# Optimization experiments

Measured on AMD Instinct MI355X. Metric: run time of the kernel, lower is better.

The kernel has to match this reference:

```python
import jax, jax.numpy as jnp
import numpy as np

NEG_SLOPE = 0.2  # PyG GATConv default LeakyReLU slope


def _gat_layer(x, src, dst, W, a_src, a_dst, b, n_nodes):
    # x: [N, Fin]; W: [Fin, H*C]; a_src/a_dst: [H, C]; b: [H*C]
    H, C = a_src.shape
    h = (x @ W).reshape(n_nodes, H, C)            # [N,H,C]
    e_s = jnp.einsum('nhc,hc->nh', h, a_src)      # [N,H]
    e_d = jnp.einsum('nhc,hc->nh', h, a_dst)
    e = jax.nn.leaky_relu(e_s[src] + e_d[dst], NEG_SLOPE)   # [E,H]
    # segment softmax over edges grouped by destination node
    m = jax.ops.segment_max(e, dst, num_segments=n_nodes)   # [N,H]
    ex = jnp.exp(e - m[dst])
    denom = jax.ops.segment_sum(ex, dst, num_segments=n_nodes)
    coef = ex / denom[dst]                         # [E,H]
    out = jax.ops.segment_sum(h[src] * coef[:, :, None], dst, num_segments=n_nodes)
    return out.reshape(n_nodes, H * C) + b         # concat=True


def _xavier(key, shape):
    fan_in, fan_out = shape[0], shape[-1]
    lim = float(np.sqrt(6.0 / (fan_in + fan_out)))
    return jax.random.uniform(key, shape, jnp.float32, -lim, lim)


def setup_inputs() -> dict:
    key = jax.random.key(0)
    ks = jax.random.split(key, 24)
    N, E, Fin, G = 50000, 1600000, 128, 64
    x = jax.random.normal(ks[0], (N, Fin), jnp.float32)
    edge_index = jax.random.randint(ks[1], (2, E), 0, N, jnp.int64)
    batch = jnp.sort(jax.random.randint(ks[2], (N,), 0, G, jnp.int64))
    # (Fin, H, C) per layer
    cfg = [(128, 1, 32), (32, 2, 32), (64, 2, 64), (128, 2, 32), (64, 2, 8)]
    params = {}
    i = 3
    for li, (fi, H, C) in enumerate(cfg, 1):
        params[f'W{li}'] = _xavier(ks[i], (fi, H * C)); i += 1
        params[f'as{li}'] = _xavier(ks[i], (H, C)) ; i += 1
        params[f'ad{li}'] = _xavier(ks[i], (H, C)) ; i += 1
        params[f'b{li}'] = jnp.zeros((H * C,), jnp.float32)
    params['fcW'] = _xavier(ks[20], (16, 1))
    params['fcb'] = jnp.zeros((1,), jnp.float32)
    return dict(x=x, edge_index=edge_index, batch=batch, **params)


def reference(x, edge_index, batch,
              W1, as1, ad1, b1, W2, as2, ad2, b2, W3, as3, ad3, b3,
              W4, as4, ad4, b4, W5, as5, ad5, b5, fcW, fcb):
    N = x.shape[0]
    G = 64
    # add self-loops (PyG GATConv default add_self_loops=True)
    loop = jnp.arange(N, dtype=edge_index.dtype)
    src = jnp.concatenate([edge_index[0], loop])
    dst = jnp.concatenate([edge_index[1], loop])
    h = jax.nn.relu(_gat_layer(x, src, dst, W1, as1, ad1, b1, N))
    h = jax.nn.relu(_gat_layer(h, src, dst, W2, as2, ad2, b2, N))
    h = jax.nn.relu(_gat_layer(h, src, dst, W3, as3, ad3, b3, N))
    h = jax.nn.relu(_gat_layer(h, src, dst, W4, as4, ad4, b4, N))
    h = jax.nn.relu(_gat_layer(h, src, dst, W5, as5, ad5, b5, N))
    # global mean pool over graphs (dropout is identity at inference)
    sums = jax.ops.segment_sum(h, batch, num_segments=G)          # [G,16]
    cnt = jax.ops.segment_sum(jnp.ones((N,), h.dtype), batch, num_segments=G)
    pooled = sums / jnp.maximum(cnt, 1.0)[:, None]
    return jax.nn.sigmoid(pooled @ fcW + fcb)                     # [G,1]
```

## Files before the change

kernel.cpp:

```cpp
#include <hip/hip_runtime.h>
#include <math.h>

#define TPB 256
#define NEG_SLOPE 0.2f
#define EPB 2048
#define BK 512

static inline int cdiv_l(long a, int b){ return (int)((a + b - 1) / b); }

typedef float v2f __attribute__((ext_vector_type(2)));

__device__ __forceinline__ ushort f2bf(float f){
  unsigned u = __float_as_uint(f);
  unsigned r = u + 0x7fffu + ((u >> 16) & 1u);
  return (ushort)(r >> 16);
}
__device__ __forceinline__ float bf2f(unsigned hi16){ return __uint_as_float(hi16 << 16); }
__device__ __forceinline__ unsigned pbf2(float a, float b){
  return (unsigned)f2bf(a) | ((unsigned)f2bf(b) << 16);
}

template<int Fin, int HC, int C, typename XT>
__global__ __launch_bounds__(256) void gemm2_k(const XT* __restrict__ X,
        const float* __restrict__ W, const float* __restrict__ as_,
        const float* __restrict__ ad_, float* __restrict__ es, float* __restrict__ ed,
        unsigned char* __restrict__ Hb, int N){
  constexpr int TPN = HC / 4;
  constexpr int NPB = 256 / TPN;
  constexpr int H   = HC / C;
  constexpr int RG  = C / 4;
  __shared__ float Wl[Fin * HC];
  for (int i = threadIdx.x; i < Fin * HC; i += 256) Wl[i] = W[i];
  __syncthreads();
  const int t  = threadIdx.x;
  const int n  = blockIdx.x * NPB + t / TPN;
  const int jt = (t % TPN) * 4;
  if (n >= N) return;
  const XT* xr = X + (size_t)n * Fin;
  float acc[4] = {0.f, 0.f, 0.f, 0.f};
  for (int k = 0; k < Fin; k += 4){
    float xv[4];
    if constexpr (sizeof(XT) == 4){
      float4 v = *(const float4*)(xr + k);
      xv[0] = v.x; xv[1] = v.y; xv[2] = v.z; xv[3] = v.w;
    } else {
      uint2 u = *(const uint2*)(xr + k);
      xv[0] = bf2f(u.x & 0xffffu); xv[1] = bf2f(u.x >> 16);
      xv[2] = bf2f(u.y & 0xffffu); xv[3] = bf2f(u.y >> 16);
    }
#pragma unroll
    for (int kk = 0; kk < 4; ++kk){
#pragma unroll
      for (int j = 0; j < 4; ++j)
        acc[j] = fmaf(xv[kk], Wl[(k + kk) * HC + jt + j], acc[j]);
    }
  }
  int pk8 = __builtin_amdgcn_cvt_pk_fp8_f32(acc[0], acc[1], 0, false);
  pk8     = __builtin_amdgcn_cvt_pk_fp8_f32(acc[2], acc[3], pk8, true);
  *(int*)(Hb + (size_t)n * HC + jt) = pk8;
  const int head = jt / C, col = jt % C;
  float ps = 0.f, pd = 0.f;
#pragma unroll
  for (int j = 0; j < 4; ++j){
    ps = fmaf(acc[j], as_[head * C + col + j], ps);
    pd = fmaf(acc[j], ad_[head * C + col + j], pd);
  }
#pragma unroll
  for (int off = RG >> 1; off >= 1; off >>= 1){
    ps += __shfl_xor(ps, off);
    pd += __shfl_xor(pd, off);
  }
  if ((t % RG) == 0){
    es[n * H + head] = ps;
    ed[n * H + head] = pd;
  }
}


__global__ __launch_bounds__(256) void bucket_hist_k(const int* __restrict__ dst,
                        int* __restrict__ bcount, int E){
  __shared__ int lh[128];
  const int t = threadIdx.x;
  for (int i = t; i < 128; i += TPB) lh[i] = 0;
  __syncthreads();
  const int c0 = blockIdx.x * EPB;
  int i1 = c0 + EPB; if (i1 > E) i1 = E;
  for (int i = c0 + t; i < i1; i += TPB)
    atomicAdd(&lh[dst[i] >> 9], 1);
  __syncthreads();
  for (int i = t; i < 128; i += TPB)
    if (lh[i]) atomicAdd(&bcount[i], lh[i]);
}

__global__ void bucket_scan_k(const int* __restrict__ bcount,
                              int* __restrict__ bbase, int* __restrict__ bcur, int K){
  __shared__ int v[128];
  const int t = threadIdx.x;
  int orig = (t < K) ? bcount[t] : 0;
  v[t] = orig; __syncthreads();
  for (int off = 1; off < 128; off <<= 1){
    int y = (t >= off) ? v[t - off] : 0;
    __syncthreads();
    v[t] += y;
    __syncthreads();
  }
  int excl = v[t] - orig;
  if (t < K){ bbase[t] = excl; bcur[t] = excl; }
}

__global__ __launch_bounds__(256) void partition_k(const int* __restrict__ src,
                        const int* __restrict__ dst,
                        int* __restrict__ bcur, unsigned* __restrict__ packed, int E){
  __shared__ int lh[128];
  __shared__ int lofs[128];
  const int t = threadIdx.x;
  for (int i = t; i < 128; i += TPB) lh[i] = 0;
  __syncthreads();
  const int c0 = blockIdx.x * EPB;
  int i1 = c0 + EPB; if (i1 > E) i1 = E;
  for (int i = c0 + t; i < i1; i += TPB)
    atomicAdd(&lh[dst[i] >> 9], 1);
  __syncthreads();
  if (t < 128){
    lofs[t] = lh[t] ? atomicAdd(&bcur[t], lh[t]) : 0;
    lh[t] = 0;
  }
  __syncthreads();
  for (int i = c0 + t; i < i1; i += TPB){
    int d = dst[i], k = d >> 9;
    int r = atomicAdd(&lh[k], 1);
    packed[lofs[k] + r] = ((unsigned)src[i] << 9) | (unsigned)(d & 511);
  }
}

__global__ __launch_bounds__(256) void bucket_csr_k(const unsigned* __restrict__ packed,
                        const int* __restrict__ bbase, const int* __restrict__ bcur,
                        int* __restrict__ row_off, int* __restrict__ csr_src,
                        int N, int E, int K){
  __shared__ int hist[BK];
  __shared__ int cur[BK];
  __shared__ int scan2[256];
  const int k = blockIdx.x;
  const int t = threadIdx.x;
  const int b0 = bbase[k], b1 = bcur[k];
  const int nb = k * BK;
  int nloc = N - nb; if (nloc > BK) nloc = BK;

  for (int i = t; i < BK; i += 256) hist[i] = 0;
  __syncthreads();
  for (int i = b0 + t; i < b1; i += 256)
    atomicAdd(&hist[packed[i] & 511u], 1);
  __syncthreads();

  int a0 = hist[2 * t], a1 = hist[2 * t + 1];
  int pair = a0 + a1;
  scan2[t] = pair; __syncthreads();
  for (int off = 1; off < 256; off <<= 1){
    int y = (t >= off) ? scan2[t - off] : 0;
    __syncthreads();
    scan2[t] += y;
    __syncthreads();
  }
  int pexcl = scan2[t] - pair;
  const int base = b0 + nb;
  int i0 = 2 * t, i1n = 2 * t + 1;
  if (i0 < nloc){
    int r = base + pexcl + i0;
    row_off[nb + i0] = r;
    csr_src[r] = nb + i0;
    cur[i0] = r + 1;
  }
  if (i1n < nloc){
    int r = base + pexcl + a0 + i1n;
    row_off[nb + i1n] = r;
    csr_src[r] = nb + i1n;
    cur[i1n] = r + 1;
  }
  if (k == K - 1 && t == 0) row_off[N] = E + N;
  __syncthreads();

  for (int i = b0 + t; i < b1; i += 256){
    unsigned pk = packed[i];
    int p = atomicAdd(&cur[pk & 511u], 1);
    csr_src[p] = (int)(pk >> 9);
  }
}


template<int H, int C>
__global__ __launch_bounds__(256) void agg_k(const int* __restrict__ csr_src,
        const int* __restrict__ row_off,
        const float* __restrict__ es, const float* __restrict__ ed,
        const unsigned char* __restrict__ Hb, const float* __restrict__ b,
        ushort* __restrict__ outp, int N){
  constexpr int HC  = H * C;
  constexpr int LPE = HC / 8;
  constexpr int EPW = 64 / LPE;
  const int lane = threadIdx.x & 63;
  const int wv   = threadIdx.x >> 6;
  const int n = blockIdx.x * 4 + wv;
  if (n >= N) return;
  const int beg = row_off[n];
  const int deg = row_off[n + 1] - beg;

  const int grp  = lane / LPE;
  const int cpos = lane % LPE;
  const int c0   = cpos * 8;
  const int hd   = c0 / C;

  float edn[H];
#pragma unroll
  for (int h = 0; h < H; ++h) edn[h] = ed[n * H + h];

  float den[H];
#pragma unroll
  for (int h = 0; h < H; ++h) den[h] = 0.f;
  float acc[8] = {0.f,0.f,0.f,0.f,0.f,0.f,0.f,0.f};

  for (int base = 0; base < deg; base += 64){
    int j = base + lane;
    float t0f = 0.f; unsigned tpk = 0; int sidx = 0;
    if (j < deg){
      sidx = csr_src[beg + j];
      if (H == 2){
        float2 e2 = *(const float2*)(es + sidx * 2);
        float ea = e2.x + edn[0];
        ea = ea > 0.f ? ea : ea * NEG_SLOPE;
        ea = fminf(ea, 80.f);
        float ta = __expf(ea);
        float eb = e2.y + edn[1];
        eb = eb > 0.f ? eb : eb * NEG_SLOPE;
        eb = fminf(eb, 80.f);
        float tb = __expf(eb);
        den[0] += ta; den[1] += tb;
        tpk = pbf2(ta, tb);
      } else {
        float e = es[sidx] + edn[0];
        e = e > 0.f ? e : e * NEG_SLOPE;
        e = fminf(e, 80.f);
        t0f = __expf(e);
        den[0] += t0f;
      }
    }
    int cnt = deg - base; if (cnt > 64) cnt = 64;

    int i = 0;
    for (; i + EPW < cnt; i += 2 * EPW){
      int sl0 = i + grp, sl1 = sl0 + EPW;
      int sj0 = __shfl(sidx, sl0);
      int sj1 = __shfl(sidx, sl1);
      float tf0, tf1;
      if (H == 2){
        unsigned w0 = (unsigned)__shfl((int)tpk, sl0);
        unsigned w1 = (unsigned)__shfl((int)tpk, sl1);
        tf0 = bf2f(hd ? (w0 >> 16) : (w0 & 0xffffu));
        tf1 = bf2f(hd ? (w1 >> 16) : (w1 & 0xffffu));
      } else {
        tf0 = __shfl(t0f, sl0);
        tf1 = __shfl(t0f, sl1);
      }
      const unsigned char* hr0 = Hb + (size_t)sj0 * HC + c0;
      const unsigned char* hr1 = Hb + (size_t)sj1 * HC + c0;
      uint2 v0 = *(const uint2*)hr0;
      uint2 v1 = *(const uint2*)hr1;
      v2f p0 = __builtin_amdgcn_cvt_pk_f32_fp8((int)v0.x, false);
      v2f p1 = __builtin_amdgcn_cvt_pk_f32_fp8((int)v0.x, true);
      v2f p2 = __builtin_amdgcn_cvt_pk_f32_fp8((int)v0.y, false);
      v2f p3 = __builtin_amdgcn_cvt_pk_f32_fp8((int)v0.y, true);
      acc[0] = fmaf(tf0, p0[0], acc[0]); acc[1] = fmaf(tf0, p0[1], acc[1]);
      acc[2] = fmaf(tf0, p1[0], acc[2]); acc[3] = fmaf(tf0, p1[1], acc[3]);
      acc[4] = fmaf(tf0, p2[0], acc[4]); acc[5] = fmaf(tf0, p2[1], acc[5]);
      acc[6] = fmaf(tf0, p3[0], acc[6]); acc[7] = fmaf(tf0, p3[1], acc[7]);
      v2f q0 = __builtin_amdgcn_cvt_pk_f32_fp8((int)v1.x, false);
      v2f q1 = __builtin_amdgcn_cvt_pk_f32_fp8((int)v1.x, true);
      v2f q2 = __builtin_amdgcn_cvt_pk_f32_fp8((int)v1.y, false);
      v2f q3 = __builtin_amdgcn_cvt_pk_f32_fp8((int)v1.y, true);
      acc[0] = fmaf(tf1, q0[0], acc[0]); acc[1] = fmaf(tf1, q0[1], acc[1]);
      acc[2] = fmaf(tf1, q1[0], acc[2]); acc[3] = fmaf(tf1, q1[1], acc[3]);
      acc[4] = fmaf(tf1, q2[0], acc[4]); acc[5] = fmaf(tf1, q2[1], acc[5]);
      acc[6] = fmaf(tf1, q3[0], acc[6]); acc[7] = fmaf(tf1, q3[1], acc[7]);
    }
    for (; i < cnt; i += EPW){
      int sl = i + grp;
      int sj = __shfl(sidx, sl);
      float tf;
      if (H == 2){
        unsigned w = (unsigned)__shfl((int)tpk, sl);
        tf = bf2f(hd ? (w >> 16) : (w & 0xffffu));
      } else {
        tf = __shfl(t0f, sl);
      }
      const unsigned char* hr = Hb + (size_t)sj * HC + c0;
      uint2 v = *(const uint2*)hr;
      v2f p0 = __builtin_amdgcn_cvt_pk_f32_fp8((int)v.x, false);
      v2f p1 = __builtin_amdgcn_cvt_pk_f32_fp8((int)v.x, true);
      v2f p2 = __builtin_amdgcn_cvt_pk_f32_fp8((int)v.y, false);
      v2f p3 = __builtin_amdgcn_cvt_pk_f32_fp8((int)v.y, true);
      acc[0] = fmaf(tf, p0[0], acc[0]); acc[1] = fmaf(tf, p0[1], acc[1]);
      acc[2] = fmaf(tf, p1[0], acc[2]); acc[3] = fmaf(tf, p1[1], acc[3]);
      acc[4] = fmaf(tf, p2[0], acc[4]); acc[5] = fmaf(tf, p2[1], acc[5]);
      acc[6] = fmaf(tf, p3[0], acc[6]); acc[7] = fmaf(tf, p3[1], acc[7]);
    }
  }

  float sinv[H];
#pragma unroll
  for (int h = 0; h < H; ++h){
    float v = den[h];
#pragma unroll
    for (int off = 32; off >= 1; off >>= 1) v += __shfl_xor(v, off);
    sinv[h] = 1.f / v;
  }

#pragma unroll
  for (int off = LPE; off < 64; off <<= 1){
#pragma unroll
    for (int k = 0; k < 8; ++k) acc[k] += __shfl_xor(acc[k], off);
  }

  if (grp == 0){
    float si = sinv[hd];
    float o[8];
#pragma unroll
    for (int k = 0; k < 8; ++k){
      float v = fmaf(acc[k], si, b[c0 + k]);
      o[k] = v > 0.f ? v : 0.f;
    }
    uint4 w;
    w.x = pbf2(o[0], o[1]); w.y = pbf2(o[2], o[3]);
    w.z = pbf2(o[4], o[5]); w.w = pbf2(o[6], o[7]);
    *(uint4*)(outp + (size_t)n * HC + c0) = w;
  }
}


__global__ __launch_bounds__(256) void pool_k(const ushort* __restrict__ f,
                       const int* __restrict__ batch,
                       float* __restrict__ pooled, float* __restrict__ cnt, int N){
  __shared__ float sp[64 * 16];
  __shared__ float sc[64];
  const int t = threadIdx.x;
  for (int i = t; i < 64 * 16; i += 256) sp[i] = 0.f;
  for (int i = t; i < 64; i += 256) sc[i] = 0.f;
  __syncthreads();
  const int per = (N + gridDim.x - 1) / gridDim.x;
  const int n0 = blockIdx.x * per;
  int n1 = n0 + per; if (n1 > N) n1 = N;
  const int nloc = t >> 4, c = t & 15;
  for (int n = n0 + nloc; n < n1; n += 16){
    int g = batch[n];
    atomicAdd(&sp[g * 16 + c], bf2f(f[(size_t)n * 16 + c]));
    if (c == 0) atomicAdd(&sc[g], 1.f);
  }
  __syncthreads();
  for (int i = t; i < 64 * 16; i += 256) if (sp[i] != 0.f) atomicAdd(&pooled[i], sp[i]);
  for (int i = t; i < 64; i += 256)      if (sc[i] != 0.f) atomicAdd(&cnt[i], sc[i]);
}

__global__ void final_fc_k(const float* __restrict__ pooled, const float* __restrict__ cnt,
                           const float* __restrict__ fcW, const float* __restrict__ fcb,
                           float* __restrict__ outp){
  int g = threadIdx.x;
  if (g >= 64) return;
  float c = cnt[g]; c = c > 1.f ? c : 1.f;
  float inv = 1.0f / c;
  float acc = fcb[0];
  for (int i = 0; i < 16; ++i) acc = fmaf(pooled[g * 16 + i] * inv, fcW[i], acc);
  outp[g] = 1.0f / (1.0f + expf(-acc));
}


extern "C" void kernel_launch(void* const* d_in, const int* in_sizes, int n_in,
                              void* d_out, int out_size, void* d_ws, size_t ws_size,
                              hipStream_t stream) {
  const float* x    = (const float*)d_in[0];
  const int*  ei    = (const int*)d_in[1];
  const int*  batch = (const int*)d_in[2];

  const int N = in_sizes[0] / 128;
  const int E = in_sizes[1] / 2;

  const int* src = ei;
  const int* dst = ei + E;

  const float* W_[5];  const float* as_[5]; const float* ad_[5]; const float* b_[5];
  for (int l = 0; l < 5; ++l) {
    W_[l]  = (const float*)d_in[3 + 4 * l + 0];
    as_[l] = (const float*)d_in[3 + 4 * l + 1];
    ad_[l] = (const float*)d_in[3 + 4 * l + 2];
    b_[l]  = (const float*)d_in[3 + 4 * l + 3];
  }
  const float* fcW = (const float*)d_in[23];
  const float* fcb = (const float*)d_in[24];
  float* outp = (float*)d_out;

  ushort*        f_buf  = (ushort*)d_ws;
  unsigned char* Hb     = (unsigned char*)(f_buf + (size_t)N * 128);
  float*         es     = (float*)(Hb + (size_t)N * 128);
  float*         ed     = es + (size_t)N * 2;
  float*         pooled = ed + (size_t)N * 2;
  float*         cnt    = pooled + 64 * 16;
  int*           bcount = (int*)(cnt + 64);
  int*           bbase  = bcount + 128;
  int*           bcur   = bbase + 128;
  int*           row_off= bcur + 128;
  int*           csr_src= row_off + N + 1;
  unsigned*      packed = (unsigned*)(csr_src + E + N);

  const int K    = (N + BK - 1) / BK;
  const int nch  = cdiv_l(E, EPB);

  hipMemsetAsync(bcount, 0, 128 * 4, stream);
  bucket_hist_k<<<nch, TPB, 0, stream>>>(dst, bcount, E);
  bucket_scan_k<<<1, 128, 0, stream>>>(bcount, bbase, bcur, K);
  partition_k<<<nch, TPB, 0, stream>>>(src, dst, bcur, packed, E);
  bucket_csr_k<<<K, 256, 0, stream>>>(packed, bbase, bcur, row_off, csr_src, N, E, K);

  const int gb = cdiv_l(N, 4);

  gemm2_k<128,32,32,float><<<cdiv_l(N, 1024/32), 256, 0, stream>>>(x, W_[0], as_[0], ad_[0], es, ed, Hb, N);
  agg_k<1,32><<<gb, 256, 0, stream>>>(csr_src, row_off, es, ed, Hb, b_[0], f_buf, N);
  gemm2_k<32,64,32,ushort><<<cdiv_l(N, 1024/64), 256, 0, stream>>>(f_buf, W_[1], as_[1], ad_[1], es, ed, Hb, N);
  agg_k<2,32><<<gb, 256, 0, stream>>>(csr_src, row_off, es, ed, Hb, b_[1], f_buf, N);
  gemm2_k<64,128,64,ushort><<<cdiv_l(N, 1024/128), 256, 0, stream>>>(f_buf, W_[2], as_[2], ad_[2], es, ed, Hb, N);
  agg_k<2,64><<<gb, 256, 0, stream>>>(csr_src, row_off, es, ed, Hb, b_[2], f_buf, N);
  gemm2_k<128,64,32,ushort><<<cdiv_l(N, 1024/64), 256, 0, stream>>>(f_buf, W_[3], as_[3], ad_[3], es, ed, Hb, N);
  agg_k<2,32><<<gb, 256, 0, stream>>>(csr_src, row_off, es, ed, Hb, b_[3], f_buf, N);
  gemm2_k<64,16,8,ushort><<<cdiv_l(N, 1024/16), 256, 0, stream>>>(f_buf, W_[4], as_[4], ad_[4], es, ed, Hb, N);
  agg_k<2,8><<<gb, 256, 0, stream>>>(csr_src, row_off, es, ed, Hb, b_[4], f_buf, N);

  hipMemsetAsync(pooled, 0, (64 * 16 + 64) * 4, stream);
  pool_k<<<64, 256, 0, stream>>>(f_buf, batch, pooled, cnt, N);
  final_fc_k<<<1, 64, 0, stream>>>(pooled, cnt, fcW, fcb, outp);
}
```

Measured before the change: 345.2 us.

## Register-block GEMM over four nodes and stage aggregation edge data in LDS

The projection GEMM kernel now computes four nodes per thread, so each weight value read from shared memory feeds four FMAs, and each block covers four times as many nodes. The aggregation kernel writes each lane's source index and attention weight into a per-wave shared-memory array and reads them back, replacing the per-edge shuffles. It also drops the scalar tail loop: leftover slots carry zero weight and source 0, so the loop always processes edge pairs. The cost is extra LDS traffic, higher register pressure in the GEMM, and some wasted gathers of row 0 on ragged tails.

After: 349.6 us. No clear change (+1.3%).

```diff
diff --git a/kernel.cpp b/kernel.cpp
--- a/kernel.cpp
+++ b/kernel.cpp
@@ -26,53 +26,84 @@
         const float* __restrict__ ad_, float* __restrict__ es, float* __restrict__ ed,
         unsigned char* __restrict__ Hb, int N){
   constexpr int TPN = HC / 4;
-  constexpr int NPB = 256 / TPN;
+  constexpr int NPB = (256 / TPN) * 4;
   constexpr int H   = HC / C;
   constexpr int RG  = C / 4;
   __shared__ float Wl[Fin * HC];
   for (int i = threadIdx.x; i < Fin * HC; i += 256) Wl[i] = W[i];
   __syncthreads();
   const int t  = threadIdx.x;
-  const int n  = blockIdx.x * NPB + t / TPN;
-  const int jt = (t % TPN) * 4;
-  if (n >= N) return;
-  const XT* xr = X + (size_t)n * Fin;
-  float acc[4] = {0.f, 0.f, 0.f, 0.f};
+  const int cg = t % TPN;
+  const int ng = t / TPN;
+  const int jt = cg * 4;
+  const int nb = blockIdx.x * NPB + ng * 4;
+  const XT* xr[4];
+#pragma unroll
+  for (int m = 0; m < 4; ++m)
+    xr[m] = X + (size_t)((nb + m < N) ? nb + m : 0) * Fin;
+
+  float acc[4][4];
+#pragma unroll
+  for (int m = 0; m < 4; ++m)
+#pragma unroll
+    for (int j = 0; j < 4; ++j) acc[m][j] = 0.f;
+
   for (int k = 0; k < Fin; k += 4){
-    float xv[4];
-    if constexpr (sizeof(XT) == 4){
-      float4 v = *(const float4*)(xr + k);
-      xv[0] = v.x; xv[1] = v.y; xv[2] = v.z; xv[3] = v.w;
-    } else {
-      uint2 u = *(const uint2*)(xr + k);
-      xv[0] = bf2f(u.x & 0xffffu); xv[1] = bf2f(u.x >> 16);
-      xv[2] = bf2f(u.y & 0xffffu); xv[3] = bf2f(u.y >> 16);
+    float xv[4][4];
+#pragma unroll
+    for (int m = 0; m < 4; ++m){
+      if constexpr (sizeof(XT) == 4){
+        float4 v = *(const float4*)(xr[m] + k);
+        xv[m][0] = v.x; xv[m][1] = v.y; xv[m][2] = v.z; xv[m][3] = v.w;
+      } else {
+        uint2 u = *(const uint2*)(xr[m] + k);
+        xv[m][0] = bf2f(u.x & 0xffffu); xv[m][1] = bf2f(u.x >> 16);
+        xv[m][2] = bf2f(u.y & 0xffffu); xv[m][3] = bf2f(u.y >> 16);
+      }
     }
 #pragma unroll
     for (int kk = 0; kk < 4; ++kk){
-#pragma unroll
-      for (int j = 0; j < 4; ++j)
-        acc[j] = fmaf(xv[kk], Wl[(k + kk) * HC + jt + j], acc[j]);
-    }
-  }
-  int pk8 = __builtin_amdgcn_cvt_pk_fp8_f32(acc[0], acc[1], 0, false);
-  pk8     = __builtin_amdgcn_cvt_pk_fp8_f32(acc[2], acc[3], pk8, true);
-  *(int*)(Hb + (size_t)n * HC + jt) = pk8;
-  const int head = jt / C, col = jt % C;
-  float ps = 0.f, pd = 0.f;
-#pragma unroll
-  for (int j = 0; j < 4; ++j){
-    ps = fmaf(acc[j], as_[head * C + col + j], ps);
-    pd = fmaf(acc[j], ad_[head * C + col + j], pd);
-  }
-#pragma unroll
-  for (int off = RG >> 1; off >= 1; off >>= 1){
-    ps += __shfl_xor(ps, off);
-    pd += __shfl_xor(pd, off);
-  }
-  if ((t % RG) == 0){
-    es[n * H + head] = ps;
-    ed[n * H + head] = pd;
+      float w0 = Wl[(k + kk) * HC + jt + 0];
+      float w1 = Wl[(k + kk) * HC + jt + 1];
+      float w2 = Wl[(k + kk) * HC + jt + 2];
+      float w3 = Wl[(k + kk) * HC + jt + 3];
+#pragma unroll
+      for (int m = 0; m < 4; ++m){
+        acc[m][0] = fmaf(xv[m][kk], w0, acc[m][0]);
+        acc[m][1] = fmaf(xv[m][kk], w1, acc[m][1]);
+        acc[m][2] = fmaf(xv[m][kk], w2, acc[m][2]);
+        acc[m][3] = fmaf(xv[m][kk], w3, acc[m][3]);
+      }
+    }
+  }
+
+  const int head = jt / C;
+  const float* asp = as_ + head * C + (jt % C);
+  const float* adp = ad_ + head * C + (jt % C);
+#pragma unroll
+  for (int m = 0; m < 4; ++m){
+    int n = nb + m;
+    bool v = (n < N);
+    if (v){
+      int pk8 = __builtin_amdgcn_cvt_pk_fp8_f32(acc[m][0], acc[m][1], 0, false);
+      pk8     = __builtin_amdgcn_cvt_pk_fp8_f32(acc[m][2], acc[m][3], pk8, true);
+      *(int*)(Hb + (size_t)n * HC + jt) = pk8;
+    }
+    float ps = 0.f, pd = 0.f;
+#pragma unroll
+    for (int j = 0; j < 4; ++j){
+      ps = fmaf(acc[m][j], asp[j], ps);
+      pd = fmaf(acc[m][j], adp[j], pd);
+    }
+#pragma unroll
+    for (int off = RG >> 1; off >= 1; off >>= 1){
+      ps += __shfl_xor(ps, off);
+      pd += __shfl_xor(pd, off);
+    }
+    if (v && (cg % RG) == 0){
+      es[n * H + head] = ps;
+      ed[n * H + head] = pd;
+    }
   }
 }
 
@@ -196,6 +227,7 @@
   constexpr int HC  = H * C;
   constexpr int LPE = HC / 8;
   constexpr int EPW = 64 / LPE;
+  __shared__ uint2 stg[4][64];
   const int lane = threadIdx.x & 63;
   const int wv   = threadIdx.x >> 6;
   const int n = blockIdx.x * 4 + wv;
@@ -219,7 +251,7 @@
 
   for (int base = 0; base < deg; base += 64){
     int j = base + lane;
-    float t0f = 0.f; unsigned tpk = 0; int sidx = 0;
+    unsigned wbits = 0; int sidx = 0;
     if (j < deg){
       sidx = csr_src[beg + j];
       if (H == 2){
@@ -233,34 +265,34 @@
         eb = fminf(eb, 80.f);
         float tb = __expf(eb);
         den[0] += ta; den[1] += tb;
-        tpk = pbf2(ta, tb);
+        wbits = pbf2(ta, tb);
       } else {
         float e = es[sidx] + edn[0];
         e = e > 0.f ? e : e * NEG_SLOPE;
         e = fminf(e, 80.f);
-        t0f = __expf(e);
+        float t0f = __expf(e);
         den[0] += t0f;
+        wbits = __float_as_uint(t0f);
       }
     }
+    __asm__ volatile("s_waitcnt lgkmcnt(0)" ::: "memory");
+    stg[wv][lane] = make_uint2((unsigned)sidx, wbits);
+    __asm__ volatile("s_waitcnt lgkmcnt(0)" ::: "memory");
+
     int cnt = deg - base; if (cnt > 64) cnt = 64;
-
-    int i = 0;
-    for (; i + EPW < cnt; i += 2 * EPW){
-      int sl0 = i + grp, sl1 = sl0 + EPW;
-      int sj0 = __shfl(sidx, sl0);
-      int sj1 = __shfl(sidx, sl1);
+    for (int i = 0; i < cnt; i += 2 * EPW){
+      uint2 e0 = stg[wv][i + grp];
+      uint2 e1 = stg[wv][i + grp + EPW];
       float tf0, tf1;
       if (H == 2){
-        unsigned w0 = (unsigned)__shfl((int)tpk, sl0);
-        unsigned w1 = (unsigned)__shfl((int)tpk, sl1);
-        tf0 = bf2f(hd ? (w0 >> 16) : (w0 & 0xffffu));
-        tf1 = bf2f(hd ? (w1 >> 16) : (w1 & 0xffffu));
+        tf0 = bf2f(hd ? (e0.y >> 16) : (e0.y & 0xffffu));
+        tf1 = bf2f(hd ? (e1.y >> 16) : (e1.y & 0xffffu));
       } else {
-        tf0 = __shfl(t0f, sl0);
-        tf1 = __shfl(t0f, sl1);
+        tf0 = __uint_as_float(e0.y);
+        tf1 = __uint_as_float(e1.y);
       }
-      const unsigned char* hr0 = Hb + (size_t)sj0 * HC + c0;
-      const unsigned char* hr1 = Hb + (size_t)sj1 * HC + c0;
+      const unsigned char* hr0 = Hb + (size_t)e0.x * HC + c0;
+      const unsigned char* hr1 = Hb + (size_t)e1.x * HC + c0;
       uint2 v0 = *(const uint2*)hr0;
       uint2 v1 = *(const uint2*)hr1;
       v2f p0 = __builtin_amdgcn_cvt_pk_f32_fp8((int)v0.x, false);
@@ -280,27 +312,6 @@
       acc[4] = fmaf(tf1, q2[0], acc[4]); acc[5] = fmaf(tf1, q2[1], acc[5]);
       acc[6] = fmaf(tf1, q3[0], acc[6]); acc[7] = fmaf(tf1, q3[1], acc[7]);
     }
-    for (; i < cnt; i += EPW){
-      int sl = i + grp;
-      int sj = __shfl(sidx, sl);
-      float tf;
-      if (H == 2){
-        unsigned w = (unsigned)__shfl((int)tpk, sl);
-        tf = bf2f(hd ? (w >> 16) : (w & 0xffffu));
-      } else {
-        tf = __shfl(t0f, sl);
-      }
-      const unsigned char* hr = Hb + (size_t)sj * HC + c0;
-      uint2 v = *(const uint2*)hr;
-      v2f p0 = __builtin_amdgcn_cvt_pk_f32_fp8((int)v.x, false);
-      v2f p1 = __builtin_amdgcn_cvt_pk_f32_fp8((int)v.x, true);
-      v2f p2 = __builtin_amdgcn_cvt_pk_f32_fp8((int)v.y, false);
-      v2f p3 = __builtin_amdgcn_cvt_pk_f32_fp8((int)v.y, true);
-      acc[0] = fmaf(tf, p0[0], acc[0]); acc[1] = fmaf(tf, p0[1], acc[1]);
-      acc[2] = fmaf(tf, p1[0], acc[2]); acc[3] = fmaf(tf, p1[1], acc[3]);
-      acc[4] = fmaf(tf, p2[0], acc[4]); acc[5] = fmaf(tf, p2[1], acc[5]);
-      acc[6] = fmaf(tf, p3[0], acc[6]); acc[7] = fmaf(tf, p3[1], acc[7]);
-    }
   }
 
   float sinv[H];
@@ -418,15 +429,15 @@
 
   const int gb = cdiv_l(N, 4);
 
-  gemm2_k<128,32,32,float><<<cdiv_l(N, 1024/32), 256, 0, stream>>>(x, W_[0], as_[0], ad_[0], es, ed, Hb, N);
+  gemm2_k<128,32,32,float><<<cdiv_l(N, 4096/32), 256, 0, stream>>>(x, W_[0], as_[0], ad_[0], es, ed, Hb, N);
   agg_k<1,32><<<gb, 256, 0, stream>>>(csr_src, row_off, es, ed, Hb, b_[0], f_buf, N);
-  gemm2_k<32,64,32,ushort><<<cdiv_l(N, 1024/64), 256, 0, stream>>>(f_buf, W_[1], as_[1], ad_[1], es, ed, Hb, N);
+  gemm2_k<32,64,32,ushort><<<cdiv_l(N, 4096/64), 256, 0, stream>>>(f_buf, W_[1], as_[1], ad_[1], es, ed, Hb, N);
   agg_k<2,32><<<gb, 256, 0, stream>>>(csr_src, row_off, es, ed, Hb, b_[1], f_buf, N);
-  gemm2_k<64,128,64,ushort><<<cdiv_l(N, 1024/128), 256, 0, stream>>>(f_buf, W_[2], as_[2], ad_[2], es, ed, Hb, N);
+  gemm2_k<64,128,64,ushort><<<cdiv_l(N, 4096/128), 256, 0, stream>>>(f_buf, W_[2], as_[2], ad_[2], es, ed, Hb, N);
   agg_k<2,64><<<gb, 256, 0, stream>>>(csr_src, row_off, es, ed, Hb, b_[2], f_buf, N);
-  gemm2_k<128,64,32,ushort><<<cdiv_l(N, 1024/64), 256, 0, stream>>>(f_buf, W_[3], as_[3], ad_[3], es, ed, Hb, N);
+  gemm2_k<128,64,32,ushort><<<cdiv_l(N, 4096/64), 256, 0, stream>>>(f_buf, W_[3], as_[3], ad_[3], es, ed, Hb, N);
   agg_k<2,32><<<gb, 256, 0, stream>>>(csr_src, row_off, es, ed, Hb, b_[3], f_buf, N);
-  gemm2_k<64,16,8,ushort><<<cdiv_l(N, 1024/16), 256, 0, stream>>>(f_buf, W_[4], as_[4], ad_[4], es, ed, Hb, N);
+  gemm2_k<64,16,8,ushort><<<cdiv_l(N, 4096/16), 256, 0, stream>>>(f_buf, W_[4], as_[4], ad_[4], es, ed, Hb, N);
   agg_k<2,8><<<gb, 256, 0, stream>>>(csr_src, row_off, es, ed, Hb, b_[4], f_buf, N);
 
   hipMemsetAsync(pooled, 0, (64 * 16 + 64) * 4, stream);
```
